# Kernel tuning notes

Hardware: AMD Instinct MI355X
Metric: run time of the kernel (lower is better)

Reference implementation:

```python
import jax, jax.numpy as jnp
import numpy as np

B, C, T = 64, 384, 512
DUR_MAX = 8            # durations drawn from [0, 8)
MAX_NEW_TIME = 4096    # static padded output length >= T * (DUR_MAX - 1)


def setup_inputs() -> dict:
    key = jax.random.key(0)
    kx, kd = jax.random.split(key)
    x = jax.random.normal(kx, (B, C, T), dtype=jnp.float32)
    duration = jax.random.randint(kd, (B, 1, T), 0, DUR_MAX, dtype=jnp.int32)
    return {"x": x, "duration": duration}


def reference(x, duration):
    # x: [B, C, T] float32, duration: [B, 1, T] int32
    dur = duration[:, 0, :]                      # [B, T]
    csum = jnp.cumsum(dur, axis=-1)              # [B, T] exclusive-right cumsum boundaries
    total = csum[:, -1]                          # [B] expanded length per sample
    j = jnp.arange(MAX_NEW_TIME, dtype=jnp.int32)  # output frame positions
    # source phoneme index for each output frame: smallest t with j < csum[t]
    idx = jax.vmap(lambda c: jnp.searchsorted(c, j, side="right"))(csum)  # [B, MAX_NEW_TIME]
    idx = jnp.clip(idx, 0, T - 1)
    # gather along time, broadcast over channels -> [B, C, MAX_NEW_TIME]
    out = jnp.take_along_axis(x, idx[:, None, :].astype(jnp.int32), axis=-1)
    valid = j[None, :] < total[:, None]          # [B, MAX_NEW_TIME]
    out = jnp.where(valid[:, None, :], out, jnp.zeros((), dtype=x.dtype))
    # mask derived from non-zero values of channel 0, matching torch code
    new_mask = (out[:, 0:1, :] != 0).astype(jnp.int32)  # [B, 1, MAX_NEW_TIME]
    return out, new_mask
```

## Files before the change

### kernel.cpp

```cpp
#include <hip/hip_runtime.h>


#define BB 64
#define CC 384
#define TT 512
#define TOUT 4096
#define CB 16

__global__ __launch_bounds__(256) void length_regulator_fused(
    const float* __restrict__ x, const int* __restrict__ dur,
    float* __restrict__ out, float* __restrict__ mask) {
  const int b = blockIdx.y;
  const int c0 = blockIdx.x * CB;
  const int tid = threadIdx.x;

  __shared__ float xs[CB * TT];
  int* const idx_lds = (int*)xs;
  int* const spair   = (int*)xs + TOUT;

  const float4* __restrict__ xb4 =
      (const float4*)(x + ((size_t)b * CC + c0) * TT);
  float4 xr[CB * TT / 4 / 256];
  #pragma unroll
  for (int k = 0; k < CB * TT / 4 / 256; ++k)
    xr[k] = xb4[k * 256 + tid];

  const int2 d2 = ((const int2*)(dur + (size_t)b * TT))[tid];
  spair[tid] = d2.x + d2.y;
  #pragma unroll
  for (int k = 0; k < TOUT / 256; ++k) idx_lds[k * 256 + tid] = -1;
  __syncthreads();

  #pragma unroll
  for (int off = 1; off < 256; off <<= 1) {
    const int v = (tid >= off) ? spair[tid - off] : 0;
    __syncthreads();
    spair[tid] += v;
    __syncthreads();
  }

  const int e1 = spair[tid];
  const int s1 = e1 - d2.y;
  const int s0 = s1 - d2.x;
  for (int p = s0; p < s1; ++p) idx_lds[p] = 2 * tid;
  for (int p = s1; p < e1; ++p) idx_lds[p] = 2 * tid + 1;
  __syncthreads();

  int4 I[TOUT / 1024];
  #pragma unroll
  for (int jt = 0; jt < TOUT / 1024; ++jt)
    I[jt] = ((const int4*)idx_lds)[jt * 256 + tid];
  __syncthreads();

  float4* const xs4 = (float4*)xs;
  #pragma unroll
  for (int k = 0; k < CB * TT / 4 / 256; ++k)
    xs4[k * 256 + tid] = xr[k];
  __syncthreads();

  float* __restrict__ ob = out + ((size_t)b * CC + c0) * TOUT + tid * 4;

  #pragma unroll
  for (int jt = 0; jt < TOUT / 1024; ++jt) {
    const int4 i4 = I[jt];
    #pragma unroll
    for (int c = 0; c < CB; ++c) {
      const float* __restrict__ row = xs + c * TT;
      float4 v;
      v.x = (i4.x >= 0) ? row[i4.x] : 0.0f;
      v.y = (i4.y >= 0) ? row[i4.y] : 0.0f;
      v.z = (i4.z >= 0) ? row[i4.z] : 0.0f;
      v.w = (i4.w >= 0) ? row[i4.w] : 0.0f;
      *(float4*)(ob + (size_t)c * TOUT + jt * 1024) = v;

      if (c == 0 && c0 == 0) {
        float4 m;
        m.x = (v.x != 0.0f) ? 1.0f : 0.0f;
        m.y = (v.y != 0.0f) ? 1.0f : 0.0f;
        m.z = (v.z != 0.0f) ? 1.0f : 0.0f;
        m.w = (v.w != 0.0f) ? 1.0f : 0.0f;
        *(float4*)(mask + (size_t)b * TOUT + jt * 1024 + tid * 4) = m;
      }
    }
  }
}

extern "C" void kernel_launch(void* const* d_in, const int* in_sizes, int n_in,
                              void* d_out, int out_size, void* d_ws, size_t ws_size,
                              hipStream_t stream) {
  const float* x = (const float*)d_in[0];
  const int* dur = (const int*)d_in[1];

  float* out = (float*)d_out;
  float* mask = out + (size_t)BB * CC * TOUT;

  length_regulator_fused<<<dim3(CC / CB, BB), 256, 0, stream>>>(x, dur, out, mask);
}
```

Measured before the change: 437.0 us.

## Halve channel block, use wave-shuffle scan and nontemporal output stores

```diff
diff --git a/kernel.cpp b/kernel.cpp
--- a/kernel.cpp
+++ b/kernel.cpp
@@ -5,41 +5,48 @@
 #define CC 384
 #define TT 512
 #define TOUT 4096
-#define CB 16
+#define CB 8
 
-__global__ __launch_bounds__(256) void length_regulator_fused(
+typedef float f32x4 __attribute__((ext_vector_type(4)));
+
+__global__ __launch_bounds__(256) void length_regulator_v3(
     const float* __restrict__ x, const int* __restrict__ dur,
     float* __restrict__ out, float* __restrict__ mask) {
   const int b = blockIdx.y;
   const int c0 = blockIdx.x * CB;
   const int tid = threadIdx.x;
+  const int lane = tid & 63;
+  const int w = tid >> 6;
 
   __shared__ float xs[CB * TT];
+  __shared__ int wsum[4];
   int* const idx_lds = (int*)xs;
-  int* const spair   = (int*)xs + TOUT;
 
-  const float4* __restrict__ xb4 =
-      (const float4*)(x + ((size_t)b * CC + c0) * TT);
-  float4 xr[CB * TT / 4 / 256];
+  const f32x4* __restrict__ xb4 =
+      (const f32x4*)(x + ((size_t)b * CC + c0) * TT);
+  f32x4 xr[CB * TT / 4 / 256];
   #pragma unroll
   for (int k = 0; k < CB * TT / 4 / 256; ++k)
     xr[k] = xb4[k * 256 + tid];
 
   const int2 d2 = ((const int2*)(dur + (size_t)b * TT))[tid];
-  spair[tid] = d2.x + d2.y;
+  int ps = d2.x + d2.y;
+  #pragma unroll
+  for (int off = 1; off < 64; off <<= 1) {
+    const int v = __shfl_up(ps, off);
+    if (lane >= off) ps += v;
+  }
+
   #pragma unroll
   for (int k = 0; k < TOUT / 256; ++k) idx_lds[k * 256 + tid] = -1;
+  if (lane == 63) wsum[w] = ps;
   __syncthreads();
 
-  #pragma unroll
-  for (int off = 1; off < 256; off <<= 1) {
-    const int v = (tid >= off) ? spair[tid - off] : 0;
-    __syncthreads();
-    spair[tid] += v;
-    __syncthreads();
-  }
-
-  const int e1 = spair[tid];
+  int prefix = 0;
+  if (w > 0) prefix += wsum[0];
+  if (w > 1) prefix += wsum[1];
+  if (w > 2) prefix += wsum[2];
+  const int e1 = ps + prefix;
   const int s1 = e1 - d2.y;
   const int s0 = s1 - d2.x;
   for (int p = s0; p < s1; ++p) idx_lds[p] = 2 * tid;
@@ -52,7 +59,7 @@
     I[jt] = ((const int4*)idx_lds)[jt * 256 + tid];
   __syncthreads();
 
-  float4* const xs4 = (float4*)xs;
+  f32x4* const xs4 = (f32x4*)xs;
   #pragma unroll
   for (int k = 0; k < CB * TT / 4 / 256; ++k)
     xs4[k * 256 + tid] = xr[k];
@@ -66,20 +73,22 @@
     #pragma unroll
     for (int c = 0; c < CB; ++c) {
       const float* __restrict__ row = xs + c * TT;
-      float4 v;
+      f32x4 v;
       v.x = (i4.x >= 0) ? row[i4.x] : 0.0f;
       v.y = (i4.y >= 0) ? row[i4.y] : 0.0f;
       v.z = (i4.z >= 0) ? row[i4.z] : 0.0f;
       v.w = (i4.w >= 0) ? row[i4.w] : 0.0f;
-      *(float4*)(ob + (size_t)c * TOUT + jt * 1024) = v;
+      __builtin_nontemporal_store(
+          v, (f32x4*)(ob + (size_t)c * TOUT + jt * 1024));
 
       if (c == 0 && c0 == 0) {
-        float4 m;
+        f32x4 m;
         m.x = (v.x != 0.0f) ? 1.0f : 0.0f;
         m.y = (v.y != 0.0f) ? 1.0f : 0.0f;
         m.z = (v.z != 0.0f) ? 1.0f : 0.0f;
         m.w = (v.w != 0.0f) ? 1.0f : 0.0f;
-        *(float4*)(mask + (size_t)b * TOUT + jt * 1024 + tid * 4) = m;
+        __builtin_nontemporal_store(
+            m, (f32x4*)(mask + (size_t)b * TOUT + jt * 1024 + tid * 4));
       }
     }
   }
@@ -94,5 +103,5 @@
   float* out = (float*)d_out;
   float* mask = out + (size_t)BB * CC * TOUT;
 
-  length_regulator_fused<<<dim3(CC / CB, BB), 256, 0, stream>>>(x, dur, out, mask);
+  length_regulator_v3<<<dim3(CC / CB, BB), 256, 0, stream>>>(x, dur, out, mask);
 }
```

After: 432.1 us. About the same (-1.1%).
